# Optimization experiments

Hardware: AMD Instinct MI355X
Metric: run time of the kernel (lower is better)

The kernel has to match this reference:

```python
import jax, jax.numpy as jnp
import numpy as np

HIDDEN = 256
HEADS = 8
HEAD_DIM = HIDDEN // HEADS
SCALE = HEAD_DIM ** -0.5


def setup_inputs() -> dict:
    key = jax.random.key(0)
    ks = jax.random.split(key, 12)
    B, N = 2, 2048
    s = lambda fan_in: 1.0 / np.sqrt(fan_in)
    inp = {
        'x': jax.random.normal(ks[0], (B, N, HIDDEN), jnp.float32),
        'coords': jax.random.normal(ks[1], (B, N, 3), jnp.float32),
        'W_qkv': jax.random.normal(ks[2], (HIDDEN, 3 * HIDDEN), jnp.float32) * s(HIDDEN),
        'W_out': jax.random.normal(ks[3], (HIDDEN, HIDDEN), jnp.float32) * s(HIDDEN),
        'b_out': jnp.zeros((HIDDEN,), jnp.float32),
        'pos_w1': jax.random.normal(ks[4], (3, 16), jnp.float32) * s(3),
        'pos_b1': jnp.zeros((16,), jnp.float32),
        'pos_w2': jax.random.normal(ks[5], (16, HEADS), jnp.float32) * s(16),
        'pos_b2': jnp.zeros((HEADS,), jnp.float32),
        'sym_w1': jax.random.normal(ks[6], (3, 16), jnp.float32) * s(3),
        'sym_b1': jnp.zeros((16,), jnp.float32),
        'sym_w2': jax.random.normal(ks[7], (16, HEADS), jnp.float32) * s(16),
        'sym_b2': jnp.zeros((HEADS,), jnp.float32),
    }
    return inp


def _bias_mlp(rel, w1, b1, w2, b2):
    # rel: [B,N,N,3] -> [B,H,N,N]
    h = jax.nn.relu(jnp.einsum('bijc,ck->bijk', rel, w1) + b1)
    out = jnp.einsum('bijk,kh->bijh', h, w2) + b2
    return jnp.transpose(out, (0, 3, 1, 2))


def reference(x, coords, W_qkv, W_out, b_out, pos_w1, pos_b1, pos_w2, pos_b2,
              sym_w1, sym_b1, sym_w2, sym_b2):
    B, N, C = x.shape
    qkv = (x @ W_qkv).reshape(B, N, 3, HEADS, HEAD_DIM)
    qkv = jnp.transpose(qkv, (2, 0, 3, 1, 4))  # [3,B,H,N,D]
    q, k, v = qkv[0], qkv[1], qkv[2]
    dots = jnp.einsum('bhid,bhjd->bhij', q, k) * SCALE
    rel_pos = coords[:, :, None, :] - coords[:, None, :, :]  # [B,N,N,3]
    reflect = jnp.array([-1.0, 1.0, 1.0], dtype=coords.dtype)
    coords_sym = coords * reflect
    sym_rel_pos = coords[:, :, None, :] - coords_sym[:, None, :, :]
    bias_direct = _bias_mlp(rel_pos, pos_w1, pos_b1, pos_w2, pos_b2)
    bias_sym = _bias_mlp(sym_rel_pos, sym_w1, sym_b1, sym_w2, sym_b2)
    attn = jax.nn.softmax(dots + bias_direct + bias_sym, axis=-1)
    out = jnp.einsum('bhij,bhjd->bhid', attn, v)
    out = jnp.transpose(out, (0, 2, 1, 3)).reshape(B, N, C)
    return out @ W_out + b_out
```

## Files before the change

kernel.cpp:

```cpp
#include <hip/hip_runtime.h>
#include <hip/hip_fp16.h>

typedef _Float16 half8_t __attribute__((ext_vector_type(8)));
typedef _Float16 half4_t __attribute__((ext_vector_type(4)));
typedef _Float16 h2      __attribute__((ext_vector_type(2)));
typedef float    f32x4   __attribute__((ext_vector_type(4)));

#define LOG2E 1.4426950408889634f
#define KSCALE (0.17677669529663687f * LOG2E)

#if __has_builtin(__builtin_amdgcn_exp2f)
#define EXP2F(x) __builtin_amdgcn_exp2f(x)
#else
#define EXP2F(x) exp2f(x)
#endif

template <int N>
__device__ __forceinline__ int dpp_ror(int v) {
  return __builtin_amdgcn_update_dpp(0, v, 0x120 + N, 0xf, 0xf, true);
}
__device__ __forceinline__ h2 rowmax16_h2(h2 v) {
  int t;
  t = dpp_ror<1>(__builtin_bit_cast(int, v));
  v = __builtin_elementwise_max(v, __builtin_bit_cast(h2, t));
  t = dpp_ror<2>(__builtin_bit_cast(int, v));
  v = __builtin_elementwise_max(v, __builtin_bit_cast(h2, t));
  t = dpp_ror<4>(__builtin_bit_cast(int, v));
  v = __builtin_elementwise_max(v, __builtin_bit_cast(h2, t));
  t = dpp_ror<8>(__builtin_bit_cast(int, v));
  v = __builtin_elementwise_max(v, __builtin_bit_cast(h2, t));
  return v;
}
__device__ __forceinline__ float rowsum16_f32(float x) {
  int t;
  t = dpp_ror<1>(__builtin_bit_cast(int, x)); x += __builtin_bit_cast(float, t);
  t = dpp_ror<2>(__builtin_bit_cast(int, x)); x += __builtin_bit_cast(float, t);
  t = dpp_ror<4>(__builtin_bit_cast(int, x)); x += __builtin_bit_cast(float, t);
  t = dpp_ror<8>(__builtin_bit_cast(int, x)); x += __builtin_bit_cast(float, t);
  return x;
}

__global__ __launch_bounds__(256) void prep_misc(
    const float* __restrict__ x, const float* __restrict__ Wqkv,
    const float* __restrict__ Wout, const float* __restrict__ coords,
    const float* __restrict__ pw1, const float* __restrict__ pb1,
    const float* __restrict__ sw1, const float* __restrict__ sb1,
    _Float16* __restrict__ xf16, _Float16* __restrict__ WqkvT,
    _Float16* __restrict__ WoutT, _Float16* __restrict__ APre,
    _Float16* __restrict__ BPre)
{
  __shared__ float tile[64][65];
  const int bi = blockIdx.x, tid = threadIdx.x;
  if (bi < 1024) {
    const int idx = bi * 256 + tid;
    f32x4 v = *reinterpret_cast<const f32x4*>(x + idx * 4);
    half4_t h;
    h[0] = (_Float16)v[0]; h[1] = (_Float16)v[1];
    h[2] = (_Float16)v[2]; h[3] = (_Float16)v[3];
    *reinterpret_cast<half4_t*>(xf16 + idx * 4) = h;
  } else if (bi < 1088) {
    const float* src; _Float16* dst; int t, W;
    if (bi < 1072) { t = bi - 1024; src = Wqkv; dst = WqkvT; W = 768; }
    else           { t = bi - 1072; src = Wout; dst = WoutT; W = 256; }
    const int nOT = W >> 6;
    const int tk = t / nOT, to = t % nOT;
    const int cx = tid & 63, ry = tid >> 6;
#pragma unroll
    for (int rr = 0; rr < 16; ++rr) {
      const int kl = rr * 4 + ry;
      tile[kl][cx] = src[(tk * 64 + kl) * W + to * 64 + cx];
    }
    __syncthreads();
#pragma unroll
    for (int rr = 0; rr < 16; ++rr) {
      const int ol = rr * 4 + ry;
      dst[(to * 64 + ol) * 256 + tk * 64 + cx] = (_Float16)tile[cx][ol];
    }
  } else {
    const int row = (bi - 1088) * 256 + tid;
    const float c0 = coords[row * 3 + 0];
    const float c1 = coords[row * 3 + 1];
    const float c2 = coords[row * 3 + 2];
#pragma unroll
    for (int k = 0; k < 16; ++k) {
      float a = c0 * pw1[k] + c1 * pw1[16 + k] + c2 * pw1[32 + k];
      APre[row * 32 + k] = (_Float16)(a + pb1[k]);
      BPre[row * 32 + k] = (_Float16)a;
      float s  =  c0 * sw1[k] + c1 * sw1[16 + k] + c2 * sw1[32 + k];
      float sb = -c0 * sw1[k] + c1 * sw1[16 + k] + c2 * sw1[32 + k];
      APre[row * 32 + 16 + k] = (_Float16)(s + sb1[k]);
      BPre[row * 32 + 16 + k] = (_Float16)sb;
    }
  }
}

__global__ __launch_bounds__(256) void qkv_gemm(
    const _Float16* __restrict__ xf16, const _Float16* __restrict__ WqkvT,
    _Float16* __restrict__ Qh, _Float16* __restrict__ Kh,
    _Float16* __restrict__ Vt)
{
  const int wg = blockIdx.x * 4 + (threadIdx.x >> 6);
  const int ti = wg / 12, og = wg % 12;
  const int i0 = ti * 16, o0 = og * 64;
  const int lane = threadIdx.x & 63, q = lane >> 4, c = lane & 15;
  f32x4 acc[4] = {{0,0,0,0},{0,0,0,0},{0,0,0,0},{0,0,0,0}};
  const _Float16* arow = xf16 + (i0 + c) * 256;
  const _Float16* brow = WqkvT + (o0 + c) * 256;
#pragma unroll
  for (int k0 = 0; k0 < 256; k0 += 32) {
    half8_t af = *reinterpret_cast<const half8_t*>(arow + k0 + q * 8);
#pragma unroll
    for (int t = 0; t < 4; ++t) {
      half8_t bf = *reinterpret_cast<const half8_t*>(brow + t * 16 * 256 + k0 + q * 8);
      acc[t] = __builtin_amdgcn_mfma_f32_16x16x32_f16(af, bf, acc[t], 0, 0, 0);
    }
  }
#pragma unroll
  for (int t = 0; t < 4; ++t) {
    const int o = o0 + t * 16 + c;
    const int which = o >> 8, h = (o >> 5) & 7, d = o & 31;
#pragma unroll
    for (int r = 0; r < 4; ++r) {
      const int i = i0 + q * 4 + r;
      const int b = i >> 11, n = i & 2047;
      _Float16 v = (_Float16)acc[t][r];
      if (which == 0)      Qh[((b * 8 + h) * 2048 + n) * 32 + d] = v;
      else if (which == 1) Kh[((b * 8 + h) * 2048 + n) * 32 + d] = v;
      else                 Vt[((b * 8 + h) * 32 + d) * 2048 + n] = v;
    }
  }
}

__global__ __launch_bounds__(512, 4) void flash(
    const _Float16* __restrict__ Qh, const _Float16* __restrict__ Kh,
    const _Float16* __restrict__ Vt, const _Float16* __restrict__ APre,
    const _Float16* __restrict__ BPre, const float* __restrict__ pw2,
    const float* __restrict__ sw2, _Float16* __restrict__ Opart,
    float* __restrict__ Mpart)
{
  __shared__ __align__(16) unsigned char smem[57600];
  _Float16* biasH = reinterpret_cast<_Float16*>(smem);
  _Float16* pbuf  = reinterpret_cast<_Float16*>(smem + 37120);

  const int blk = blockIdx.x;
  const int b     = blk >> 8;
  const int chunk = (blk >> 6) & 3;
  const int i0    = (blk & 63) << 5;
  const int tid = threadIdx.x;
  const int w = tid >> 6, lane = tid & 63;
  const int q = lane >> 4, c = lane & 15;

  const _Float16* qbase = Qh + ((b * 8 + w) * 2048 + i0) * 32;
  half8_t qfA = *reinterpret_cast<const half8_t*>(qbase + c * 32 + q * 8);
  half8_t qfB = *reinterpret_cast<const half8_t*>(qbase + (16 + c) * 32 + q * 8);
  const _Float16* abase = APre + (b * 2048 + i0) * 32;
  half8_t apfA = *reinterpret_cast<const half8_t*>(abase + c * 32 + q * 8);
  half8_t apfB = *reinterpret_cast<const half8_t*>(abase + (16 + c) * 32 + q * 8);

  half8_t w2f;
#pragma unroll
  for (int jj = 0; jj < 8; ++jj) {
    const int k = q * 8 + jj;
    float val = 0.f;
    if (c < 8) val = (k < 16 ? pw2[k * 8 + c] : sw2[(k - 16) * 8 + c]) * LOG2E;
    w2f[jj] = (_Float16)val;
  }

  float mA[4], lpA[4], mB[4], lpB[4];
  f32x4 O0A = {0,0,0,0}, O1A = {0,0,0,0}, O0B = {0,0,0,0}, O1B = {0,0,0,0};
#pragma unroll
  for (int r = 0; r < 4; ++r) {
    mA[r] = -INFINITY; lpA[r] = 0.f;
    mB[r] = -INFINITY; lpB[r] = 0.f;
  }

  const f32x4 z4 = {0.f, 0.f, 0.f, 0.f};
  half8_t hzero8 = {};

  const int jbase = chunk * 512;
  const _Float16* BPre_b = BPre + (long)b * 2048 * 32;
  _Float16* pbA = pbuf + w * 1280;
  _Float16* pbB = pbA + 640;

  for (int jt = 0; jt < 16; ++jt) {
    const int j0 = jbase + jt * 32;
    _Float16* bW = biasH + (jt & 1) * 9280;

#pragma unroll
    for (int mt = 0; mt < 4; ++mt) {
      const int jl = w * 4 + mt;
      half8_t bpf = *reinterpret_cast<const half8_t*>(
          BPre_b + (j0 + jl) * 32 + q * 8);
      half8_t hvA = __builtin_elementwise_max(apfA - bpf, hzero8);
      f32x4 bcA = __builtin_amdgcn_mfma_f32_16x16x32_f16(hvA, w2f, z4, 0, 0, 0);
      half8_t hvB = __builtin_elementwise_max(apfB - bpf, hzero8);
      f32x4 bcB = __builtin_amdgcn_mfma_f32_16x16x32_f16(hvB, w2f, z4, 0, 0, 0);
      if (c < 8) {
        half4_t b4;
        b4[0] = (_Float16)bcA[0]; b4[1] = (_Float16)bcA[1];
        b4[2] = (_Float16)bcA[2]; b4[3] = (_Float16)bcA[3];
        *reinterpret_cast<half4_t*>(bW + c * 1160 + jl * 36 + q * 4) = b4;
        half4_t b5;
        b5[0] = (_Float16)bcB[0]; b5[1] = (_Float16)bcB[1];
        b5[2] = (_Float16)bcB[2]; b5[3] = (_Float16)bcB[3];
        *reinterpret_cast<half4_t*>(bW + c * 1160 + jl * 36 + 16 + q * 4) = b5;
      }
    }

    const _Float16* kbase = Kh + ((b * 8 + w) * 2048 + j0) * 32;
    half8_t kf0 = *reinterpret_cast<const half8_t*>(kbase + (2 * c) * 32 + q * 8);
    half8_t kf1 = *reinterpret_cast<const half8_t*>(kbase + (2 * c + 1) * 32 + q * 8);
    const _Float16* vbase = Vt + (b * 8 + w) * 65536 + j0;
    half8_t vf0 = *reinterpret_cast<const half8_t*>(vbase + c * 2048 + q * 8);
    half8_t vf1 = *reinterpret_cast<const half8_t*>(vbase + (16 + c) * 2048 + q * 8);
    f32x4 sA0 = __builtin_amdgcn_mfma_f32_16x16x32_f16(qfA, kf0, z4, 0, 0, 0);
    f32x4 sA1 = __builtin_amdgcn_mfma_f32_16x16x32_f16(qfA, kf1, z4, 0, 0, 0);
    f32x4 sB0 = __builtin_amdgcn_mfma_f32_16x16x32_f16(qfB, kf0, z4, 0, 0, 0);
    f32x4 sB1 = __builtin_amdgcn_mfma_f32_16x16x32_f16(qfB, kf1, z4, 0, 0, 0);

    __syncthreads();

    const _Float16* bR = biasH + (jt & 1) * 9280 + w * 1160;
    half4_t bbA0 = *reinterpret_cast<const half4_t*>(bR + (2 * c) * 36 + q * 4);
    half4_t bbA1 = *reinterpret_cast<const half4_t*>(bR + (2 * c + 1) * 36 + q * 4);
    half4_t bbB0 = *reinterpret_cast<const half4_t*>(bR + (2 * c) * 36 + 16 + q * 4);
    half4_t bbB1 = *reinterpret_cast<const half4_t*>(bR + (2 * c + 1) * 36 + 16 + q * 4);

    {
      float sv0[4], sv1[4];
      h2 pk01, pk23;
      float mr[4];
#pragma unroll
      for (int r = 0; r < 4; ++r) {
        sv0[r] = sA0[r] * KSCALE + (float)bbA0[r];
        sv1[r] = sA1[r] * KSCALE + (float)bbA1[r];
        mr[r] = fmaxf(sv0[r], sv1[r]);
      }
      pk01[0] = (_Float16)mr[0]; pk01[1] = (_Float16)mr[1];
      pk23[0] = (_Float16)mr[2]; pk23[1] = (_Float16)mr[3];
      pk01 = rowmax16_h2(pk01);
      pk23 = rowmax16_h2(pk23);
      float mred[4] = {(float)pk01[0], (float)pk01[1], (float)pk23[0], (float)pk23[1]};
#pragma unroll
      for (int r = 0; r < 4; ++r) {
        const float mnew = fmaxf(mA[r], mred[r]);
        const float alpha = EXP2F(mA[r] - mnew);
        const float p0 = EXP2F(sv0[r] - mnew);
        const float p1 = EXP2F(sv1[r] - mnew);
        lpA[r] = lpA[r] * alpha + (p0 + p1);
        mA[r] = mnew;
        O0A[r] *= alpha; O1A[r] *= alpha;
        h2 pp; pp[0] = (_Float16)p0; pp[1] = (_Float16)p1;
        *reinterpret_cast<h2*>(pbA + (q * 4 + r) * 40 + 2 * c) = pp;
      }
    }
    {
      float sv0[4], sv1[4];
      h2 pk01, pk23;
      float mr[4];
#pragma unroll
      for (int r = 0; r < 4; ++r) {
        sv0[r] = sB0[r] * KSCALE + (float)bbB0[r];
        sv1[r] = sB1[r] * KSCALE + (float)bbB1[r];
        mr[r] = fmaxf(sv0[r], sv1[r]);
      }
      pk01[0] = (_Float16)mr[0]; pk01[1] = (_Float16)mr[1];
      pk23[0] = (_Float16)mr[2]; pk23[1] = (_Float16)mr[3];
      pk01 = rowmax16_h2(pk01);
      pk23 = rowmax16_h2(pk23);
      float mred[4] = {(float)pk01[0], (float)pk01[1], (float)pk23[0], (float)pk23[1]};
#pragma unroll
      for (int r = 0; r < 4; ++r) {
        const float mnew = fmaxf(mB[r], mred[r]);
        const float alpha = EXP2F(mB[r] - mnew);
        const float p0 = EXP2F(sv0[r] - mnew);
        const float p1 = EXP2F(sv1[r] - mnew);
        lpB[r] = lpB[r] * alpha + (p0 + p1);
        mB[r] = mnew;
        O0B[r] *= alpha; O1B[r] *= alpha;
        h2 pp; pp[0] = (_Float16)p0; pp[1] = (_Float16)p1;
        *reinterpret_cast<h2*>(pbB + (q * 4 + r) * 40 + 2 * c) = pp;
      }
    }
    __threadfence_block();
    half8_t pfA = *reinterpret_cast<const half8_t*>(pbA + c * 40 + q * 8);
    half8_t pfB = *reinterpret_cast<const half8_t*>(pbB + c * 40 + q * 8);
    O0A = __builtin_amdgcn_mfma_f32_16x16x32_f16(pfA, vf0, O0A, 0, 0, 0);
    O1A = __builtin_amdgcn_mfma_f32_16x16x32_f16(pfA, vf1, O1A, 0, 0, 0);
    O0B = __builtin_amdgcn_mfma_f32_16x16x32_f16(pfB, vf0, O0B, 0, 0, 0);
    O1B = __builtin_amdgcn_mfma_f32_16x16x32_f16(pfB, vf1, O1B, 0, 0, 0);
  }

#pragma unroll
  for (int r = 0; r < 4; ++r) {
    const float s = rowsum16_f32(lpA[r]);
    const float inv = 1.f / s;
    const int n = i0 + q * 4 + r;
    const long base = (long)(((chunk * 2 + b) * 8 + w) * 2048 + n);
    Opart[base * 32 + c]      = (_Float16)(O0A[r] * inv);
    Opart[base * 32 + 16 + c] = (_Float16)(O1A[r] * inv);
    if (c == 0) Mpart[base] = mA[r] + __log2f(s);
  }
#pragma unroll
  for (int r = 0; r < 4; ++r) {
    const float s = rowsum16_f32(lpB[r]);
    const float inv = 1.f / s;
    const int n = i0 + 16 + q * 4 + r;
    const long base = (long)(((chunk * 2 + b) * 8 + w) * 2048 + n);
    Opart[base * 32 + c]      = (_Float16)(O0B[r] * inv);
    Opart[base * 32 + 16 + c] = (_Float16)(O1B[r] * inv);
    if (c == 0) Mpart[base] = mB[r] + __log2f(s);
  }
}

__global__ __launch_bounds__(256) void combine(
    const _Float16* __restrict__ Opart, const float* __restrict__ Mpart,
    _Float16* __restrict__ attnF16)
{
  const int idx = blockIdx.x * 256 + threadIdx.x;
  const int dg = idx & 3;
  const int h  = (idx >> 2) & 7;
  const int n  = (idx >> 5) & 2047;
  const int b  = idx >> 16;
  float mv[4], M = -INFINITY;
#pragma unroll
  for (int ck = 0; ck < 4; ++ck) {
    mv[ck] = Mpart[((ck * 2 + b) * 8 + h) * 2048 + n];
    M = fmaxf(M, mv[ck]);
  }
  float num[8] = {0,0,0,0,0,0,0,0};
  float den = 0.f;
#pragma unroll
  for (int ck = 0; ck < 4; ++ck) {
    const float wgt = EXP2F(mv[ck] - M);
    half8_t ov = *reinterpret_cast<const half8_t*>(
        Opart + (long)(((ck * 2 + b) * 8 + h) * 2048 + n) * 32 + dg * 8);
#pragma unroll
    for (int e = 0; e < 8; ++e) num[e] += wgt * (float)ov[e];
    den += wgt;
  }
  const float inv = 1.f / den;
  half8_t o;
#pragma unroll
  for (int e = 0; e < 8; ++e) o[e] = (_Float16)(num[e] * inv);
  *reinterpret_cast<half8_t*>(attnF16 + ((b * 2048 + n) * 256 + h * 32 + dg * 8)) = o;
}

__global__ __launch_bounds__(256) void proj(
    const _Float16* __restrict__ attnF16, const _Float16* __restrict__ WoutT,
    const float* __restrict__ bout, float* __restrict__ out)
{
  const int i0 = blockIdx.x * 16;
  const int o0 = (threadIdx.x >> 6) * 64;
  const int lane = threadIdx.x & 63, q = lane >> 4, c = lane & 15;
  f32x4 acc[4] = {{0,0,0,0},{0,0,0,0},{0,0,0,0},{0,0,0,0}};
  const _Float16* arow = attnF16 + (i0 + c) * 256;
  const _Float16* brow = WoutT + (o0 + c) * 256;
#pragma unroll
  for (int k0 = 0; k0 < 256; k0 += 32) {
    half8_t af = *reinterpret_cast<const half8_t*>(arow + k0 + q * 8);
#pragma unroll
    for (int t = 0; t < 4; ++t) {
      half8_t bf = *reinterpret_cast<const half8_t*>(brow + t * 16 * 256 + k0 + q * 8);
      acc[t] = __builtin_amdgcn_mfma_f32_16x16x32_f16(af, bf, acc[t], 0, 0, 0);
    }
  }
#pragma unroll
  for (int t = 0; t < 4; ++t) {
    const float bo = bout[o0 + t * 16 + c];
#pragma unroll
    for (int r = 0; r < 4; ++r)
      out[(i0 + q * 4 + r) * 256 + o0 + t * 16 + c] = acc[t][r] + bo;
  }
}

extern "C" void kernel_launch(void* const* d_in, const int* in_sizes, int n_in,
                              void* d_out, int out_size, void* d_ws, size_t ws_size,
                              hipStream_t stream)
{
  const float* x      = (const float*)d_in[0];
  const float* coords = (const float*)d_in[1];
  const float* Wqkv   = (const float*)d_in[2];
  const float* Wout   = (const float*)d_in[3];
  const float* bout   = (const float*)d_in[4];
  const float* pw1    = (const float*)d_in[5];
  const float* pb1    = (const float*)d_in[6];
  const float* pw2    = (const float*)d_in[7];
  const float* sw1    = (const float*)d_in[9];
  const float* sb1    = (const float*)d_in[10];
  const float* sw2    = (const float*)d_in[11];
  float* out = (float*)d_out;

  char* ws = (char*)d_ws;
  _Float16* Qh      = (_Float16*)(ws + 0);
  _Float16* Kh      = (_Float16*)(ws + 2097152);
  _Float16* Vt      = (_Float16*)(ws + 4194304);
  _Float16* xf16    = (_Float16*)(ws + 6291456);
  _Float16* attnF16 = (_Float16*)(ws + 6291456);
  _Float16* WqkvT   = (_Float16*)(ws + 8388608);
  _Float16* WoutT   = (_Float16*)(ws + 8781824);
  _Float16* APre    = (_Float16*)(ws + 8912896);
  _Float16* BPre    = (_Float16*)(ws + 9175040);
  _Float16* Opart   = (_Float16*)(ws + 9437184);
  float*    Mpart   = (float*)   (ws + 17825792);

  prep_misc<<<1104, 256, 0, stream>>>(x, Wqkv, Wout, coords, pw1, pb1, sw1, sb1,
                                      xf16, WqkvT, WoutT, APre, BPre);
  qkv_gemm<<<768, 256, 0, stream>>>(xf16, WqkvT, Qh, Kh, Vt);
  flash<<<512, 512, 0, stream>>>(Qh, Kh, Vt, APre, BPre, pw2, sw2, Opart, Mpart);
  combine<<<512, 256, 0, stream>>>(Opart, Mpart, attnF16);
  proj<<<256, 256, 0, stream>>>(attnF16, WoutT, bout, out);
}
```

Before: 183.3 us.

## Use lazy softmax rescaling in flash loop and fuse combine with output projection

The flash kernel's online softmax now computes exponentials against the running max first. It rescales the accumulators only when some lane's row max grows by more than a threshold, tested with a wave-wide vote, and the running max starts at zero instead of negative infinity. This removes the per-tile alpha exponent and the rescale multiplies from the common path. Separately, the split-K combine and the output projection are merged into one kernel that stages the combined attention rows in shared memory, removing a launch and a global round trip. The deferred rescale lets the unnormalized probabilities reach up to about 2^4 times the true max before rescaling, which adds some fp16 precision risk.

```diff
diff --git a/kernel.cpp b/kernel.cpp
--- a/kernel.cpp
+++ b/kernel.cpp
@@ -170,8 +170,8 @@
   f32x4 O0A = {0,0,0,0}, O1A = {0,0,0,0}, O0B = {0,0,0,0}, O1B = {0,0,0,0};
 #pragma unroll
   for (int r = 0; r < 4; ++r) {
-    mA[r] = -INFINITY; lpA[r] = 0.f;
-    mB[r] = -INFINITY; lpB[r] = 0.f;
+    mA[r] = 0.f; lpA[r] = 0.f;
+    mB[r] = 0.f; lpB[r] = 0.f;
   }
 
   const f32x4 z4 = {0.f, 0.f, 0.f, 0.f};
@@ -227,7 +227,7 @@
     half4_t bbB1 = *reinterpret_cast<const half4_t*>(bR + (2 * c + 1) * 36 + 16 + q * 4);
 
     {
-      float sv0[4], sv1[4];
+      float sv0[4], sv1[4], p0[4], p1[4];
       h2 pk01, pk23;
       float mr[4];
 #pragma unroll
@@ -235,27 +235,39 @@
         sv0[r] = sA0[r] * KSCALE + (float)bbA0[r];
         sv1[r] = sA1[r] * KSCALE + (float)bbA1[r];
         mr[r] = fmaxf(sv0[r], sv1[r]);
+      }
+#pragma unroll
+      for (int r = 0; r < 4; ++r) {
+        p0[r] = EXP2F(sv0[r] - mA[r]);
+        p1[r] = EXP2F(sv1[r] - mA[r]);
       }
       pk01[0] = (_Float16)mr[0]; pk01[1] = (_Float16)mr[1];
       pk23[0] = (_Float16)mr[2]; pk23[1] = (_Float16)mr[3];
       pk01 = rowmax16_h2(pk01);
       pk23 = rowmax16_h2(pk23);
       float mred[4] = {(float)pk01[0], (float)pk01[1], (float)pk23[0], (float)pk23[1]};
-#pragma unroll
-      for (int r = 0; r < 4; ++r) {
-        const float mnew = fmaxf(mA[r], mred[r]);
-        const float alpha = EXP2F(mA[r] - mnew);
-        const float p0 = EXP2F(sv0[r] - mnew);
-        const float p1 = EXP2F(sv1[r] - mnew);
-        lpA[r] = lpA[r] * alpha + (p0 + p1);
-        mA[r] = mnew;
-        O0A[r] *= alpha; O1A[r] *= alpha;
-        h2 pp; pp[0] = (_Float16)p0; pp[1] = (_Float16)p1;
+      float need = fmaxf(fmaxf(mred[0] - mA[0], mred[1] - mA[1]),
+                         fmaxf(mred[2] - mA[2], mred[3] - mA[3]));
+      if (__any(need > 4.0f)) {
+#pragma unroll
+        for (int r = 0; r < 4; ++r) {
+          const float mnew = fmaxf(mA[r], mred[r]);
+          const float alpha = EXP2F(mA[r] - mnew);
+          p0[r] *= alpha; p1[r] *= alpha;
+          lpA[r] *= alpha;
+          O0A[r] *= alpha; O1A[r] *= alpha;
+          mA[r] = mnew;
+        }
+      }
+#pragma unroll
+      for (int r = 0; r < 4; ++r) {
+        lpA[r] += p0[r] + p1[r];
+        h2 pp; pp[0] = (_Float16)p0[r]; pp[1] = (_Float16)p1[r];
         *reinterpret_cast<h2*>(pbA + (q * 4 + r) * 40 + 2 * c) = pp;
       }
     }
     {
-      float sv0[4], sv1[4];
+      float sv0[4], sv1[4], p0[4], p1[4];
       h2 pk01, pk23;
       float mr[4];
 #pragma unroll
@@ -263,22 +275,34 @@
         sv0[r] = sB0[r] * KSCALE + (float)bbB0[r];
         sv1[r] = sB1[r] * KSCALE + (float)bbB1[r];
         mr[r] = fmaxf(sv0[r], sv1[r]);
+      }
+#pragma unroll
+      for (int r = 0; r < 4; ++r) {
+        p0[r] = EXP2F(sv0[r] - mB[r]);
+        p1[r] = EXP2F(sv1[r] - mB[r]);
       }
       pk01[0] = (_Float16)mr[0]; pk01[1] = (_Float16)mr[1];
       pk23[0] = (_Float16)mr[2]; pk23[1] = (_Float16)mr[3];
       pk01 = rowmax16_h2(pk01);
       pk23 = rowmax16_h2(pk23);
       float mred[4] = {(float)pk01[0], (float)pk01[1], (float)pk23[0], (float)pk23[1]};
-#pragma unroll
-      for (int r = 0; r < 4; ++r) {
-        const float mnew = fmaxf(mB[r], mred[r]);
-        const float alpha = EXP2F(mB[r] - mnew);
-        const float p0 = EXP2F(sv0[r] - mnew);
-        const float p1 = EXP2F(sv1[r] - mnew);
-        lpB[r] = lpB[r] * alpha + (p0 + p1);
-        mB[r] = mnew;
-        O0B[r] *= alpha; O1B[r] *= alpha;
-        h2 pp; pp[0] = (_Float16)p0; pp[1] = (_Float16)p1;
+      float need = fmaxf(fmaxf(mred[0] - mB[0], mred[1] - mB[1]),
+                         fmaxf(mred[2] - mB[2], mred[3] - mB[3]));
+      if (__any(need > 4.0f)) {
+#pragma unroll
+        for (int r = 0; r < 4; ++r) {
+          const float mnew = fmaxf(mB[r], mred[r]);
+          const float alpha = EXP2F(mB[r] - mnew);
+          p0[r] *= alpha; p1[r] *= alpha;
+          lpB[r] *= alpha;
+          O0B[r] *= alpha; O1B[r] *= alpha;
+          mB[r] = mnew;
+        }
+      }
+#pragma unroll
+      for (int r = 0; r < 4; ++r) {
+        lpB[r] += p0[r] + p1[r];
+        h2 pp; pp[0] = (_Float16)p0[r]; pp[1] = (_Float16)p1[r];
         *reinterpret_cast<h2*>(pbB + (q * 4 + r) * 40 + 2 * c) = pp;
       }
     }
@@ -313,52 +337,64 @@
   }
 }
 
-__global__ __launch_bounds__(256) void combine(
+__global__ __launch_bounds__(256) void combine_proj(
     const _Float16* __restrict__ Opart, const float* __restrict__ Mpart,
-    _Float16* __restrict__ attnF16)
+    const _Float16* __restrict__ WoutT, const float* __restrict__ bout,
+    float* __restrict__ out)
 {
-  const int idx = blockIdx.x * 256 + threadIdx.x;
-  const int dg = idx & 3;
-  const int h  = (idx >> 2) & 7;
-  const int n  = (idx >> 5) & 2047;
-  const int b  = idx >> 16;
-  float mv[4], M = -INFINITY;
-#pragma unroll
-  for (int ck = 0; ck < 4; ++ck) {
-    mv[ck] = Mpart[((ck * 2 + b) * 8 + h) * 2048 + n];
-    M = fmaxf(M, mv[ck]);
-  }
-  float num[8] = {0,0,0,0,0,0,0,0};
-  float den = 0.f;
-#pragma unroll
-  for (int ck = 0; ck < 4; ++ck) {
-    const float wgt = EXP2F(mv[ck] - M);
-    half8_t ov = *reinterpret_cast<const half8_t*>(
-        Opart + (long)(((ck * 2 + b) * 8 + h) * 2048 + n) * 32 + dg * 8);
-#pragma unroll
-    for (int e = 0; e < 8; ++e) num[e] += wgt * (float)ov[e];
-    den += wgt;
-  }
-  const float inv = 1.f / den;
-  half8_t o;
-#pragma unroll
-  for (int e = 0; e < 8; ++e) o[e] = (_Float16)(num[e] * inv);
-  *reinterpret_cast<half8_t*>(attnF16 + ((b * 2048 + n) * 256 + h * 32 + dg * 8)) = o;
-}
-
-__global__ __launch_bounds__(256) void proj(
-    const _Float16* __restrict__ attnF16, const _Float16* __restrict__ WoutT,
-    const float* __restrict__ bout, float* __restrict__ out)
-{
+  __shared__ _Float16 aT[16][264];
   const int i0 = blockIdx.x * 16;
-  const int o0 = (threadIdx.x >> 6) * 64;
-  const int lane = threadIdx.x & 63, q = lane >> 4, c = lane & 15;
+  const int b = i0 >> 11;
+  const int n0 = i0 & 2047;
+  const int tid = threadIdx.x;
+  {
+    const int row = tid >> 4, cg = tid & 15;
+    const int n = n0 + row;
+    const int h = cg >> 1;
+    const int d0 = (cg & 1) * 16;
+    float mv[4], M = -INFINITY;
+#pragma unroll
+    for (int ck = 0; ck < 4; ++ck) {
+      mv[ck] = Mpart[((ck * 2 + b) * 8 + h) * 2048 + n];
+      M = fmaxf(M, mv[ck]);
+    }
+    float num[16];
+#pragma unroll
+    for (int e = 0; e < 16; ++e) num[e] = 0.f;
+    float den = 0.f;
+#pragma unroll
+    for (int ck = 0; ck < 4; ++ck) {
+      const float wgt = EXP2F(mv[ck] - M);
+      const _Float16* op = Opart +
+          (long)(((ck * 2 + b) * 8 + h) * 2048 + n) * 32 + d0;
+      half8_t o0v = *reinterpret_cast<const half8_t*>(op);
+      half8_t o1v = *reinterpret_cast<const half8_t*>(op + 8);
+#pragma unroll
+      for (int e = 0; e < 8; ++e) {
+        num[e]     += wgt * (float)o0v[e];
+        num[8 + e] += wgt * (float)o1v[e];
+      }
+      den += wgt;
+    }
+    const float inv = 1.f / den;
+    half8_t h0, h1;
+#pragma unroll
+    for (int e = 0; e < 8; ++e) {
+      h0[e] = (_Float16)(num[e] * inv);
+      h1[e] = (_Float16)(num[8 + e] * inv);
+    }
+    *reinterpret_cast<half8_t*>(&aT[row][cg * 16])     = h0;
+    *reinterpret_cast<half8_t*>(&aT[row][cg * 16 + 8]) = h1;
+  }
+  __syncthreads();
+
+  const int o0 = (tid >> 6) * 64;
+  const int lane = tid & 63, q = lane >> 4, c = lane & 15;
   f32x4 acc[4] = {{0,0,0,0},{0,0,0,0},{0,0,0,0},{0,0,0,0}};
-  const _Float16* arow = attnF16 + (i0 + c) * 256;
   const _Float16* brow = WoutT + (o0 + c) * 256;
 #pragma unroll
   for (int k0 = 0; k0 < 256; k0 += 32) {
-    half8_t af = *reinterpret_cast<const half8_t*>(arow + k0 + q * 8);
+    half8_t af = *reinterpret_cast<const half8_t*>(&aT[c][k0 + q * 8]);
 #pragma unroll
     for (int t = 0; t < 4; ++t) {
       half8_t bf = *reinterpret_cast<const half8_t*>(brow + t * 16 * 256 + k0 + q * 8);
@@ -396,7 +432,6 @@
   _Float16* Kh      = (_Float16*)(ws + 2097152);
   _Float16* Vt      = (_Float16*)(ws + 4194304);
   _Float16* xf16    = (_Float16*)(ws + 6291456);
-  _Float16* attnF16 = (_Float16*)(ws + 6291456);
   _Float16* WqkvT   = (_Float16*)(ws + 8388608);
   _Float16* WoutT   = (_Float16*)(ws + 8781824);
   _Float16* APre    = (_Float16*)(ws + 8912896);
@@ -408,6 +443,5 @@
                                       xf16, WqkvT, WoutT, APre, BPre);
   qkv_gemm<<<768, 256, 0, stream>>>(xf16, WqkvT, Qh, Kh, Vt);
   flash<<<512, 512, 0, stream>>>(Qh, Kh, Vt, APre, BPre, pw2, sw2, Opart, Mpart);
-  combine<<<512, 256, 0, stream>>>(Opart, Mpart, attnF16);
-  proj<<<256, 256, 0, stream>>>(attnF16, WoutT, bout, out);
-}
+  combine_proj<<<256, 256, 0, stream>>>(Opart, Mpart, WoutT, bout, out);
+}
```

Result: faster. 179.1 us (-2.3%).
